# Kernel tuning notes

Measured on AMD Instinct MI355X. Metric: run time of the kernel, lower is better.

Reference implementation:

```python
import jax, jax.numpy as jnp
import numpy as np

ALPHA = 0.2          # LeakyReLU negative slope
NEG_INF = -9e15      # mask fill value used by the torch module


def setup_inputs() -> dict:
    key = jax.random.key(0)
    k1, k2, k3, k4 = jax.random.split(key, 4)
    N, F_IN, F_OUT = 1024, 64, 64
    h = jax.random.normal(k1, (N, F_IN), dtype=jnp.float32)
    # adj > 0 marks edges; random 0/1 dense adjacency (diag not required: all-masked rows
    # softmax to uniform, matching torch semantics with the finite -9e15 fill)
    adj = jax.random.randint(k2, (N, N), 0, 2, dtype=jnp.int32)
    # xavier_uniform(gain=1.414) equivalents
    lim_W = 1.414 * np.sqrt(6.0 / (F_IN + F_OUT))
    W = jax.random.uniform(k3, (F_IN, F_OUT), minval=-lim_W, maxval=lim_W, dtype=jnp.float32)
    lim_a = 1.414 * np.sqrt(6.0 / (2 * F_OUT + 1))
    a = jax.random.uniform(k4, (2 * F_OUT, 1), minval=-lim_a, maxval=lim_a, dtype=jnp.float32)
    return {"h": h, "adj": adj, "W": W, "a": a}


def reference(h, adj, W, a):
    F_OUT = W.shape[1]
    Wh = h @ W                                   # (N, F_out)
    # a^T [Wh_i || Wh_j] decomposes: e_ij = (Wh @ a1)_i + (Wh @ a2)_j  -- same math,
    # without materializing the (N, N, 2F) concat tensor.
    a1, a2 = a[:F_OUT, 0], a[F_OUT:, 0]
    e = (Wh @ a1)[:, None] + (Wh @ a2)[None, :]  # (N, N)
    e = jax.nn.leaky_relu(e, negative_slope=ALPHA)
    scores = jnp.where(adj > 0, e, jnp.float32(NEG_INF))
    attention = jax.nn.softmax(scores, axis=1)   # dropout is identity at eval
    h_prime = attention @ Wh                     # (N, F_out)
    return jax.nn.elu(h_prime)                   # concat=True branch
```

## Files before the change

### kernel.cpp

```cpp
#include <hip/hip_runtime.h>

#define ALPHA 0.2f

constexpr int N = 1024;
constexpr int F = 64;
constexpr int TI = 4;
constexpr int NT = 1024;
constexpr int NW = NT / 64;

__global__ __launch_bounds__(256) void k1_wh(const float* __restrict__ h,
                                             const float* __restrict__ W,
                                             const float* __restrict__ a,
                                             float* __restrict__ Wh,
                                             float* __restrict__ e1,
                                             float* __restrict__ e2) {
    const int wave = threadIdx.x >> 6;
    const int lane = threadIdx.x & 63;
    const int i = blockIdx.x * 4 + wave;

    const float hv = h[i * F + lane];
    float acc = 0.f;
    #pragma unroll
    for (int k = 0; k < F; ++k) {
        acc += __shfl(hv, k) * W[k * F + lane];
    }
    Wh[i * F + lane] = acc;

    float v1 = acc * a[lane];
    float v2 = acc * a[F + lane];
    #pragma unroll
    for (int off = 32; off > 0; off >>= 1) {
        v1 += __shfl_down(v1, off);
        v2 += __shfl_down(v2, off);
    }
    if (lane == 0) {
        e1[i] = v1;
        e2[i] = v2;
    }
}

__global__ __launch_bounds__(NT) void k2_attn(const int* __restrict__ adj,
                                              const float* __restrict__ Wh,
                                              const float* __restrict__ e1,
                                              const float* __restrict__ e2,
                                              float* __restrict__ out) {
    const int i0 = blockIdx.x * TI;
    const int t = threadIdx.x;
    const int wave = t >> 6;
    const int lane = t & 63;

    __shared__ float e2s[N];
    __shared__ float e1s[TI];
    __shared__ float p[TI][N];
    __shared__ float redsum[NW][TI];
    __shared__ float accs[NW][TI][F];

    e2s[t] = e2[t];
    if (t < TI) e1s[t] = e1[i0 + t];
    __syncthreads();

    const float ev = e2s[t];
    float lsum[TI];
    #pragma unroll
    for (int r = 0; r < TI; ++r) {
        float s = e1s[r] + ev;
        s = (s > 0.f) ? s : ALPHA * s;
        const float pe = (adj[(size_t)(i0 + r) * N + t] > 0) ? __expf(s) : 0.f;
        p[r][t] = pe;
        lsum[r] = pe;
    }
    #pragma unroll
    for (int off = 32; off > 0; off >>= 1) {
        #pragma unroll
        for (int r = 0; r < TI; ++r)
            lsum[r] += __shfl_down(lsum[r], off);
    }
    if (lane == 0) {
        #pragma unroll
        for (int r = 0; r < TI; ++r) redsum[wave][r] = lsum[r];
    }
    __syncthreads();

    float a0 = 0.f, a1 = 0.f, a2 = 0.f, a3 = 0.f;
    const int j0 = wave * 64;
    #pragma unroll 4
    for (int j = j0; j < j0 + 64; j += 4) {
        const float4 p0 = *(const float4*)&p[0][j];
        const float4 p1 = *(const float4*)&p[1][j];
        const float4 p2 = *(const float4*)&p[2][j];
        const float4 p3 = *(const float4*)&p[3][j];
        #pragma unroll
        for (int u = 0; u < 4; ++u) {
            const float whv = Wh[(size_t)(j + u) * F + lane];
            a0 += (&p0.x)[u] * whv;
            a1 += (&p1.x)[u] * whv;
            a2 += (&p2.x)[u] * whv;
            a3 += (&p3.x)[u] * whv;
        }
    }
    accs[wave][0][lane] = a0;
    accs[wave][1][lane] = a1;
    accs[wave][2][lane] = a2;
    accs[wave][3][lane] = a3;
    __syncthreads();

    if (t < TI * F) {
        const int r = t >> 6;
        const int f = t & 63;
        float s = 0.f, dn = 0.f;
        #pragma unroll
        for (int w = 0; w < NW; ++w) {
            s += accs[w][r][f];
            dn += redsum[w][r];
        }
        const float hp = s / dn;
        out[(size_t)(i0 + r) * F + f] = (hp > 0.f) ? hp : expm1f(hp);
    }
}

extern "C" void kernel_launch(void* const* d_in, const int* in_sizes, int n_in,
                              void* d_out, int out_size, void* d_ws, size_t ws_size,
                              hipStream_t stream) {
    const float* h   = (const float*)d_in[0];
    const int*   adj = (const int*)d_in[1];
    const float* W   = (const float*)d_in[2];
    const float* a   = (const float*)d_in[3];
    float* out       = (float*)d_out;

    float* ws = (float*)d_ws;
    float* Wh = ws;
    float* e1 = ws + N * F;
    float* e2 = ws + N * F + N;

    k1_wh<<<256, 256, 0, stream>>>(h, W, a, Wh, e1, e2);
    k2_attn<<<N / TI, NT, 0, stream>>>(adj, Wh, e1, e2, out);
}
```

Baseline: 69.78 us.

## Fuse GAT into one kernel by reassociating W after attention aggregation

Merges the two kernels into one by reassociating the maths. e-scores are computed as h·(W a1) and h·(W a2), the attention weights are applied to raw h, and W is multiplied into the small per-row result at the end, so Wh is never materialized. This removes a kernel launch and the global round-trip for Wh/e1/e2. In exchange, every block recomputes all 1024 e2 values with wave-level shuffle reductions, which is redundant work repeated across 256 blocks. The change also slightly alters floating-point rounding order.

Result: slower. 97.64 us (+39.9%).

```diff
diff --git a/kernel.cpp b/kernel.cpp
--- a/kernel.cpp
+++ b/kernel.cpp
@@ -5,103 +5,118 @@
 constexpr int N = 1024;
 constexpr int F = 64;
 constexpr int TI = 4;
+constexpr int NB = N / TI;
 constexpr int NT = 1024;
 constexpr int NW = NT / 64;
 
-__global__ __launch_bounds__(256) void k1_wh(const float* __restrict__ h,
-                                             const float* __restrict__ W,
-                                             const float* __restrict__ a,
-                                             float* __restrict__ Wh,
-                                             float* __restrict__ e1,
-                                             float* __restrict__ e2) {
-    const int wave = threadIdx.x >> 6;
-    const int lane = threadIdx.x & 63;
-    const int i = blockIdx.x * 4 + wave;
-
-    const float hv = h[i * F + lane];
-    float acc = 0.f;
-    #pragma unroll
-    for (int k = 0; k < F; ++k) {
-        acc += __shfl(hv, k) * W[k * F + lane];
-    }
-    Wh[i * F + lane] = acc;
-
-    float v1 = acc * a[lane];
-    float v2 = acc * a[F + lane];
-    #pragma unroll
-    for (int off = 32; off > 0; off >>= 1) {
-        v1 += __shfl_down(v1, off);
-        v2 += __shfl_down(v2, off);
-    }
-    if (lane == 0) {
-        e1[i] = v1;
-        e2[i] = v2;
-    }
-}
-
-__global__ __launch_bounds__(NT) void k2_attn(const int* __restrict__ adj,
-                                              const float* __restrict__ Wh,
-                                              const float* __restrict__ e1,
-                                              const float* __restrict__ e2,
-                                              float* __restrict__ out) {
+__global__ __launch_bounds__(NT, 4) void gat_one(const float* __restrict__ h,
+                                                 const int* __restrict__ adj,
+                                                 const float* __restrict__ W,
+                                                 const float* __restrict__ a,
+                                                 float* __restrict__ out) {
     const int i0 = blockIdx.x * TI;
     const int t = threadIdx.x;
     const int wave = t >> 6;
     const int lane = t & 63;
 
+    __shared__ float w1s[F], w2s[F];
+    __shared__ float e1s[TI];
     __shared__ float e2s[N];
-    __shared__ float e1s[TI];
     __shared__ float p[TI][N];
     __shared__ float redsum[NW][TI];
     __shared__ float accs[NW][TI][F];
+    __shared__ float us[TI][F];
 
-    e2s[t] = e2[t];
-    if (t < TI) e1s[t] = e1[i0 + t];
-    __syncthreads();
+    int av[TI];
+    #pragma unroll
+    for (int r = 0; r < TI; ++r) av[r] = adj[(size_t)(i0 + r) * N + t];
 
-    const float ev = e2s[t];
-    float lsum[TI];
-    #pragma unroll
-    for (int r = 0; r < TI; ++r) {
-        float s = e1s[r] + ev;
-        s = (s > 0.f) ? s : ALPHA * s;
-        const float pe = (adj[(size_t)(i0 + r) * N + t] > 0) ? __expf(s) : 0.f;
-        p[r][t] = pe;
-        lsum[r] = pe;
-    }
-    #pragma unroll
-    for (int off = 32; off > 0; off >>= 1) {
+    {
+        const int f = t >> 4;
+        const int gq = t & 15;
+        const float4 wv  = *(const float4*)&W[f * F + gq * 4];
+        const float4 a1v = *(const float4*)&a[gq * 4];
+        const float4 a2v = *(const float4*)&a[F + gq * 4];
+        float s1 = wv.x * a1v.x + wv.y * a1v.y + wv.z * a1v.z + wv.w * a1v.w;
+        float s2 = wv.x * a2v.x + wv.y * a2v.y + wv.z * a2v.z + wv.w * a2v.w;
         #pragma unroll
-        for (int r = 0; r < TI; ++r)
-            lsum[r] += __shfl_down(lsum[r], off);
-    }
-    if (lane == 0) {
-        #pragma unroll
-        for (int r = 0; r < TI; ++r) redsum[wave][r] = lsum[r];
+        for (int off = 8; off > 0; off >>= 1) {
+            s1 += __shfl_down(s1, off);
+            s2 += __shfl_down(s2, off);
+        }
+        if (gq == 0) { w1s[f] = s1; w2s[f] = s2; }
     }
     __syncthreads();
 
-    float a0 = 0.f, a1 = 0.f, a2 = 0.f, a3 = 0.f;
-    const int j0 = wave * 64;
-    #pragma unroll 4
-    for (int j = j0; j < j0 + 64; j += 4) {
-        const float4 p0 = *(const float4*)&p[0][j];
-        const float4 p1 = *(const float4*)&p[1][j];
-        const float4 p2 = *(const float4*)&p[2][j];
-        const float4 p3 = *(const float4*)&p[3][j];
-        #pragma unroll
-        for (int u = 0; u < 4; ++u) {
-            const float whv = Wh[(size_t)(j + u) * F + lane];
-            a0 += (&p0.x)[u] * whv;
-            a1 += (&p1.x)[u] * whv;
-            a2 += (&p2.x)[u] * whv;
-            a3 += (&p3.x)[u] * whv;
+    {
+        const float w2v = w2s[lane];
+        const float w1v = w1s[lane];
+        const int jbase = wave * 64;
+        #pragma unroll 2
+        for (int s = 0; s < 64; ++s) {
+            const int j = jbase + s;
+            const float hv = h[(size_t)j * F + lane];
+            float v2 = hv * w2v;
+            #pragma unroll
+            for (int off = 32; off > 0; off >>= 1) v2 += __shfl_down(v2, off);
+            if (lane == 0) e2s[j] = v2;
+            if (j >= i0 && j < i0 + TI) {
+                float v1 = hv * w1v;
+                #pragma unroll
+                for (int off = 32; off > 0; off >>= 1) v1 += __shfl_down(v1, off);
+                if (lane == 0) e1s[j - i0] = v1;
+            }
         }
     }
-    accs[wave][0][lane] = a0;
-    accs[wave][1][lane] = a1;
-    accs[wave][2][lane] = a2;
-    accs[wave][3][lane] = a3;
+    __syncthreads();
+
+    {
+        const float ev = e2s[t];
+        float lsum[TI];
+        #pragma unroll
+        for (int r = 0; r < TI; ++r) {
+            float s = e1s[r] + ev;
+            s = (s > 0.f) ? s : ALPHA * s;
+            const float pe = (av[r] > 0) ? __expf(s) : 0.f;
+            p[r][t] = pe;
+            lsum[r] = pe;
+        }
+        #pragma unroll
+        for (int off = 32; off > 0; off >>= 1) {
+            #pragma unroll
+            for (int r = 0; r < TI; ++r)
+                lsum[r] += __shfl_down(lsum[r], off);
+        }
+        if (lane == 0) {
+            #pragma unroll
+            for (int r = 0; r < TI; ++r) redsum[wave][r] = lsum[r];
+        }
+    }
+    __syncthreads();
+
+    {
+        float a0 = 0.f, a1 = 0.f, a2 = 0.f, a3 = 0.f;
+        const int j0 = wave * 64;
+        #pragma unroll 4
+        for (int j = j0; j < j0 + 64; j += 4) {
+            const float4 p0 = *(const float4*)&p[0][j];
+            const float4 p1 = *(const float4*)&p[1][j];
+            const float4 p2 = *(const float4*)&p[2][j];
+            const float4 p3 = *(const float4*)&p[3][j];
+            #pragma unroll
+            for (int u = 0; u < 4; ++u) {
+                const float hv = h[(size_t)(j + u) * F + lane];
+                a0 += (&p0.x)[u] * hv;
+                a1 += (&p1.x)[u] * hv;
+                a2 += (&p2.x)[u] * hv;
+                a3 += (&p3.x)[u] * hv;
+            }
+        }
+        accs[wave][0][lane] = a0;
+        accs[wave][1][lane] = a1;
+        accs[wave][2][lane] = a2;
+        accs[wave][3][lane] = a3;
+    }
     __syncthreads();
 
     if (t < TI * F) {
@@ -113,8 +128,19 @@
             s += accs[w][r][f];
             dn += redsum[w][r];
         }
-        const float hp = s / dn;
-        out[(size_t)(i0 + r) * F + f] = (hp > 0.f) ? hp : expm1f(hp);
+        us[r][f] = s / dn;
+    }
+    __syncthreads();
+
+    if (t < TI * F) {
+        const int r = t >> 6;
+        const int g = t & 63;
+        float acc = 0.f;
+        #pragma unroll
+        for (int f = 0; f < F; ++f) {
+            acc += us[r][f] * W[f * F + g];
+        }
+        out[(size_t)(i0 + r) * F + g] = (acc > 0.f) ? acc : expm1f(acc);
     }
 }
 
@@ -127,11 +153,5 @@
     const float* a   = (const float*)d_in[3];
     float* out       = (float*)d_out;
 
-    float* ws = (float*)d_ws;
-    float* Wh = ws;
-    float* e1 = ws + N * F;
-    float* e2 = ws + N * F + N;
-
-    k1_wh<<<256, 256, 0, stream>>>(h, W, a, Wh, e1, e2);
-    k2_attn<<<N / TI, NT, 0, stream>>>(adj, Wh, e1, e2, out);
+    gat_one<<<NB, NT, 0, stream>>>(h, adj, W, a, out);
 }
```

## Reassociate attention matmul to skip Wh materialization and vectorize adj loads

Applied to the files above, without the earlier changes.

Uses associativity to compute e1/e2 as h·(W·a) and the output as (attention·h)·W, so the first kernel no longer builds and writes the full Wh matrix. The attention kernel now reads h directly and applies W to the four per-block rows at the end. It also changes the adjacency load to int4 per thread, issued before the first barrier. The cost is an extra per-block 4x64x64 matmul, one more barrier, and each k1e block recomputing W·a.

New measurement: 69.73 us, median of 2. Within noise of the previous version (-0.1%).

```diff
diff --git a/kernel.cpp b/kernel.cpp
--- a/kernel.cpp
+++ b/kernel.cpp
@@ -8,26 +8,38 @@
 constexpr int NT = 1024;
 constexpr int NW = NT / 64;
 
-__global__ __launch_bounds__(256) void k1_wh(const float* __restrict__ h,
-                                             const float* __restrict__ W,
-                                             const float* __restrict__ a,
-                                             float* __restrict__ Wh,
-                                             float* __restrict__ e1,
-                                             float* __restrict__ e2) {
-    const int wave = threadIdx.x >> 6;
-    const int lane = threadIdx.x & 63;
+__global__ __launch_bounds__(256) void k1e(const float* __restrict__ h,
+                                           const float* __restrict__ W,
+                                           const float* __restrict__ a,
+                                           float* __restrict__ e1,
+                                           float* __restrict__ e2) {
+    const int t = threadIdx.x;
+    __shared__ float w1s[F], w2s[F];
+
+    {
+        const int f = t >> 2;
+        const int c0 = (t & 3) * 16;
+        float s1 = 0.f, s2 = 0.f;
+        #pragma unroll
+        for (int q = 0; q < 4; ++q) {
+            const float4 wv  = *(const float4*)&W[f * F + c0 + q * 4];
+            const float4 a1v = *(const float4*)&a[c0 + q * 4];
+            const float4 a2v = *(const float4*)&a[F + c0 + q * 4];
+            s1 += wv.x*a1v.x + wv.y*a1v.y + wv.z*a1v.z + wv.w*a1v.w;
+            s2 += wv.x*a2v.x + wv.y*a2v.y + wv.z*a2v.z + wv.w*a2v.w;
+        }
+        s1 += __shfl_down(s1, 2); s1 += __shfl_down(s1, 1);
+        s2 += __shfl_down(s2, 2); s2 += __shfl_down(s2, 1);
+        if ((t & 3) == 0) { w1s[f] = s1; w2s[f] = s2; }
+    }
+    __syncthreads();
+
+    const int wave = t >> 6;
+    const int lane = t & 63;
     const int i = blockIdx.x * 4 + wave;
-
-    const float hv = h[i * F + lane];
-    float acc = 0.f;
-    #pragma unroll
-    for (int k = 0; k < F; ++k) {
-        acc += __shfl(hv, k) * W[k * F + lane];
-    }
-    Wh[i * F + lane] = acc;
-
-    float v1 = acc * a[lane];
-    float v2 = acc * a[F + lane];
+    const float hv = h[(size_t)i * F + lane];
+    float v1 = hv * w1s[lane];
+    float v2 = hv * w2s[lane];
     #pragma unroll
     for (int off = 32; off > 0; off >>= 1) {
         v1 += __shfl_down(v1, off);
@@ -39,11 +51,12 @@
     }
 }
 
-__global__ __launch_bounds__(NT) void k2_attn(const int* __restrict__ adj,
-                                              const float* __restrict__ Wh,
-                                              const float* __restrict__ e1,
-                                              const float* __restrict__ e2,
-                                              float* __restrict__ out) {
+__global__ __launch_bounds__(NT) void k2e(const int* __restrict__ adj,
+                                          const float* __restrict__ h,
+                                          const float* __restrict__ W,
+                                          const float* __restrict__ e1,
+                                          const float* __restrict__ e2,
+                                          float* __restrict__ out) {
     const int i0 = blockIdx.x * TI;
     const int t = threadIdx.x;
     const int wave = t >> 6;
@@ -52,69 +65,79 @@
     __shared__ float e2s[N];
     __shared__ float e1s[TI];
     __shared__ float p[TI][N];
-    __shared__ float redsum[NW][TI];
     __shared__ float accs[NW][TI][F];
+    __shared__ float redsum[NW];
+    __shared__ float us[TI][F];
+
+    const int r = t >> 8;
+    const int j4 = (t & 255) * 4;
+    const int4 av = *(const int4*)&adj[(size_t)(i0 + r) * N + j4];
 
     e2s[t] = e2[t];
     if (t < TI) e1s[t] = e1[i0 + t];
     __syncthreads();
 
-    const float ev = e2s[t];
-    float lsum[TI];
-    #pragma unroll
-    for (int r = 0; r < TI; ++r) {
-        float s = e1s[r] + ev;
-        s = (s > 0.f) ? s : ALPHA * s;
-        const float pe = (adj[(size_t)(i0 + r) * N + t] > 0) ? __expf(s) : 0.f;
-        p[r][t] = pe;
-        lsum[r] = pe;
-    }
-    #pragma unroll
-    for (int off = 32; off > 0; off >>= 1) {
+    {
+        const float e1r = e1s[r];
+        const float4 ev = *(const float4*)&e2s[j4];
+        float4 pe;
+        float s;
+        s = e1r + ev.x; s = (s > 0.f) ? s : ALPHA * s; pe.x = (av.x > 0) ? __expf(s) : 0.f;
+        s = e1r + ev.y; s = (s > 0.f) ? s : ALPHA * s; pe.y = (av.y > 0) ? __expf(s) : 0.f;
+        s = e1r + ev.z; s = (s > 0.f) ? s : ALPHA * s; pe.z = (av.z > 0) ? __expf(s) : 0.f;
+        s = e1r + ev.w; s = (s > 0.f) ? s : ALPHA * s; pe.w = (av.w > 0) ? __expf(s) : 0.f;
+        *(float4*)&p[r][j4] = pe;
+        float ls = (pe.x + pe.y) + (pe.z + pe.w);
         #pragma unroll
-        for (int r = 0; r < TI; ++r)
-            lsum[r] += __shfl_down(lsum[r], off);
-    }
-    if (lane == 0) {
-        #pragma unroll
-        for (int r = 0; r < TI; ++r) redsum[wave][r] = lsum[r];
+        for (int off = 32; off > 0; off >>= 1) ls += __shfl_down(ls, off);
+        if (lane == 0) redsum[wave] = ls;
     }
     __syncthreads();
 
-    float a0 = 0.f, a1 = 0.f, a2 = 0.f, a3 = 0.f;
-    const int j0 = wave * 64;
-    #pragma unroll 4
-    for (int j = j0; j < j0 + 64; j += 4) {
-        const float4 p0 = *(const float4*)&p[0][j];
-        const float4 p1 = *(const float4*)&p[1][j];
-        const float4 p2 = *(const float4*)&p[2][j];
-        const float4 p3 = *(const float4*)&p[3][j];
-        #pragma unroll
-        for (int u = 0; u < 4; ++u) {
-            const float whv = Wh[(size_t)(j + u) * F + lane];
-            a0 += (&p0.x)[u] * whv;
-            a1 += (&p1.x)[u] * whv;
-            a2 += (&p2.x)[u] * whv;
-            a3 += (&p3.x)[u] * whv;
+    {
+        float a0 = 0.f, a1 = 0.f, a2 = 0.f, a3 = 0.f;
+        const int j0 = wave * 64;
+        #pragma unroll 4
+        for (int j = j0; j < j0 + 64; j += 4) {
+            const float4 p0 = *(const float4*)&p[0][j];
+            const float4 p1 = *(const float4*)&p[1][j];
+            const float4 p2 = *(const float4*)&p[2][j];
+            const float4 p3 = *(const float4*)&p[3][j];
+            #pragma unroll
+            for (int u = 0; u < 4; ++u) {
+                const float hv = h[(size_t)(j + u) * F + lane];
+                a0 += (&p0.x)[u] * hv;
+                a1 += (&p1.x)[u] * hv;
+                a2 += (&p2.x)[u] * hv;
+                a3 += (&p3.x)[u] * hv;
+            }
         }
+        accs[wave][0][lane] = a0;
+        accs[wave][1][lane] = a1;
+        accs[wave][2][lane] = a2;
+        accs[wave][3][lane] = a3;
     }
-    accs[wave][0][lane] = a0;
-    accs[wave][1][lane] = a1;
-    accs[wave][2][lane] = a2;
-    accs[wave][3][lane] = a3;
     __syncthreads();
 
     if (t < TI * F) {
-        const int r = t >> 6;
+        const int rr = t >> 6;
         const int f = t & 63;
-        float s = 0.f, dn = 0.f;
+        float su = 0.f;
         #pragma unroll
-        for (int w = 0; w < NW; ++w) {
-            s += accs[w][r][f];
-            dn += redsum[w][r];
-        }
-        const float hp = s / dn;
-        out[(size_t)(i0 + r) * F + f] = (hp > 0.f) ? hp : expm1f(hp);
+        for (int w = 0; w < NW; ++w) su += accs[w][rr][f];
+        const float dn = redsum[4*rr] + redsum[4*rr+1] + redsum[4*rr+2] + redsum[4*rr+3];
+        us[rr][f] = su / dn;
+    }
+    __syncthreads();
+
+    if (t < TI * F) {
+        const int rr = t >> 6;
+        const int g = t & 63;
+        float acc = 0.f;
+        #pragma unroll
+        for (int f = 0; f < F; ++f)
+            acc += us[rr][f] * W[f * F + g];
+        out[(size_t)(i0 + rr) * F + g] = (acc > 0.f) ? acc : expm1f(acc);
     }
 }
 
@@ -128,10 +151,9 @@
     float* out       = (float*)d_out;
 
     float* ws = (float*)d_ws;
-    float* Wh = ws;
-    float* e1 = ws + N * F;
-    float* e2 = ws + N * F + N;
+    float* e1 = ws;
+    float* e2 = ws + N;
 
-    k1_wh<<<256, 256, 0, stream>>>(h, W, a, Wh, e1, e2);
-    k2_attn<<<N / TI, NT, 0, stream>>>(adj, Wh, e1, e2, out);
+    k1e<<<256, 256, 0, stream>>>(h, W, a, e1, e2);
+    k2e<<<N / TI, NT, 0, stream>>>(adj, h, W, e1, e2, out);
 }
```
